# Performance work log

Hardware: AMD Instinct MI355X
Metric: run time of the kernel (lower is better)

## Reference

```python
import jax, jax.numpy as jnp
import numpy as np

BATCH, IN_F, OUT_F = 8192, 2048, 2048
LN2 = float(np.log(2.0))


def setup_inputs() -> dict:
    key = jax.random.key(0)
    kx, kw = jax.random.split(key)
    x = jax.random.normal(kx, (BATCH, IN_F), dtype=jnp.float32)
    # kaiming_uniform_(a=sqrt(5)) on (OUT_F, IN_F+1): U(-1/sqrt(fan_in), 1/sqrt(fan_in))
    bound = 1.0 / np.sqrt(IN_F + 1)
    W = jax.random.uniform(kw, (OUT_F, IN_F + 1), dtype=jnp.float32,
                           minval=-bound, maxval=bound)
    W = W.at[:, -1].set(0.0)  # bias column initialized to 0
    return {"x": x, "W": W}


def reference(x, W):
    # UniversalKANNode forward, node_type='add', use_bias=True,
    # function = lshifted_softplus: f(x, w) = w * (softplus(x) - ln2)
    # Append bias ones column: (B, IN_F+1)
    xb = jnp.concatenate([x, jnp.ones((x.shape[0], 1), dtype=x.dtype)], axis=-1)
    phi = jax.nn.softplus(xb) - jnp.asarray(LN2, dtype=x.dtype)  # (B, IN_F+1)
    # sum over input dim of W[o,i] * phi[b,i]  ==  GEMM
    return jnp.einsum("bi,oi->bo", phi, W)  # (B, OUT_F)
```

## Files before the change

kernel.cpp:

```cpp
#include <hip/hip_runtime.h>

#define M_DIM 8192
#define N_DIM 2048
#define K_DIM 2048
#define LN2F 0.69314718055994530942f
#define LOG2EF 1.44269504088896340736f
#define BIAS_PHI 0.62009741f

typedef _Float16 f16x8 __attribute__((ext_vector_type(8)));
typedef float f32x4 __attribute__((ext_vector_type(4)));

__device__ __forceinline__ float softplus_m_ln2(float v) {
    float t = v * LOG2EF;
    float e = __builtin_amdgcn_exp2f(t);
    float r = (__builtin_amdgcn_logf(1.0f + e) - 1.0f) * LN2F;
    return t < 24.0f ? r : v - LN2F;
}

__global__ __launch_bounds__(256) void prep_kernel(const float* __restrict__ x,
                                                   const float* __restrict__ W,
                                                   _Float16* __restrict__ phi,
                                                   _Float16* __restrict__ Wh,
                                                   float* __restrict__ bias) {
    if (blockIdx.x < 8192) {
        size_t i = ((size_t)blockIdx.x * blockDim.x + threadIdx.x) * 8;
        float4 v0 = *(const float4*)(x + i);
        float4 v1 = *(const float4*)(x + i + 4);
        union { _Float16 h[8]; uint4 u; } pk;
        pk.h[0] = (_Float16)softplus_m_ln2(v0.x);
        pk.h[1] = (_Float16)softplus_m_ln2(v0.y);
        pk.h[2] = (_Float16)softplus_m_ln2(v0.z);
        pk.h[3] = (_Float16)softplus_m_ln2(v0.w);
        pk.h[4] = (_Float16)softplus_m_ln2(v1.x);
        pk.h[5] = (_Float16)softplus_m_ln2(v1.y);
        pk.h[6] = (_Float16)softplus_m_ln2(v1.z);
        pk.h[7] = (_Float16)softplus_m_ln2(v1.w);
        *(uint4*)(phi + i) = pk.u;
    } else {
        const int o = blockIdx.x - 8192;
        const float* row = W + (size_t)o * (K_DIM + 1) + threadIdx.x * 8;
        union { _Float16 h[8]; uint4 u; } pk;
#pragma unroll
        for (int j = 0; j < 8; ++j)
            pk.h[j] = (_Float16)row[j];
        *(uint4*)(Wh + (size_t)o * K_DIM + threadIdx.x * 8) = pk.u;
        if (threadIdx.x == 0)
            bias[o] = W[(size_t)o * (K_DIM + 1) + K_DIM] * BIAS_PHI;
    }
}

#define GLL(gp, lp)                                                                     \
    __builtin_amdgcn_global_load_lds((const __attribute__((address_space(1))) void*)(gp), \
                                     (__attribute__((address_space(3))) void*)(lp), 16, 0, 0)

__global__ __launch_bounds__(512, 2) void kan_gemm(const _Float16* __restrict__ A,
                                                   const _Float16* __restrict__ B,
                                                   const float* __restrict__ bias,
                                                   float* __restrict__ C) {
    __shared__ __align__(16) _Float16 sA[2][256 * 64];
    __shared__ __align__(16) _Float16 sB[2][256 * 64];

    const int tid  = threadIdx.x;
    const int lane = tid & 63;
    const int wv   = tid >> 6;
    const int wm   = wv >> 2;
    const int wn   = wv & 3;

    const size_t Arow0 = (size_t)blockIdx.x * 256;
    const size_t Bcol0 = (size_t)blockIdx.y * 256;

    const int r8 = lane >> 3;
    const int lc = (lane & 7) ^ r8;
    const _Float16* gA = A + (Arow0 + wv * 32 + r8) * (size_t)K_DIM + lc * 8;
    const _Float16* gB = B + (Bcol0 + wv * 32 + r8) * (size_t)K_DIM + lc * 8;

    const int lr   = lane & 15;
    const int kph0 = ((lane >> 4) ^ (lr & 7)) * 8;

    f32x4 acc[8][4];
#pragma unroll
    for (int i = 0; i < 8; ++i)
#pragma unroll
        for (int j = 0; j < 4; ++j)
            acc[i][j] = (f32x4){0.0f, 0.0f, 0.0f, 0.0f};

#pragma unroll
    for (int j = 0; j < 4; ++j)
        GLL(gA + (size_t)j * 8 * K_DIM, &sA[0][(wv * 32 + j * 8) * 64]);
#pragma unroll
    for (int j = 0; j < 4; ++j)
        GLL(gB + (size_t)j * 8 * K_DIM, &sB[0][(wv * 32 + j * 8) * 64]);
    asm volatile("s_waitcnt vmcnt(0)" ::: "memory");
    __builtin_amdgcn_s_barrier();

    f16x8 afr[4][2];
    f16x8 bfr[2][2];

    for (int t = 0; t < 32; ++t) {
        const int d = t & 1;
        const _Float16* sAd = sA[d];
        const _Float16* sBd = sB[d];
        _Float16* dA = sA[d ^ 1];
        _Float16* dB = sB[d ^ 1];
        const size_t kn = (size_t)(t + 1) * 64;
        const bool more = (t + 1) < 32;

#pragma unroll
        for (int mi = 0; mi < 4; ++mi)
#pragma unroll
            for (int kc = 0; kc < 2; ++kc)
                afr[mi][kc] = *(const f16x8*)&sAd[(wm * 128 + mi * 16 + lr) * 64 + (kph0 ^ (kc * 32))];
#pragma unroll
        for (int ni = 0; ni < 2; ++ni)
#pragma unroll
            for (int kc = 0; kc < 2; ++kc)
                bfr[ni][kc] = *(const f16x8*)&sBd[(wn * 64 + ni * 16 + lr) * 64 + (kph0 ^ (kc * 32))];
        if (more) {
            GLL(gA + kn + (size_t)0 * 8 * K_DIM, &dA[(wv * 32 + 0) * 64]);
            GLL(gA + kn + (size_t)1 * 8 * K_DIM, &dA[(wv * 32 + 8) * 64]);
        }
        __builtin_amdgcn_s_barrier();
        asm volatile("s_waitcnt lgkmcnt(0)" ::: "memory");
        __builtin_amdgcn_s_setprio(1);
#pragma unroll
        for (int kc = 0; kc < 2; ++kc)
#pragma unroll
            for (int mi = 0; mi < 4; ++mi)
#pragma unroll
                for (int ni = 0; ni < 2; ++ni)
                    acc[mi][ni] = __builtin_amdgcn_mfma_f32_16x16x32_f16(
                        afr[mi][kc], bfr[ni][kc], acc[mi][ni], 0, 0, 0);
        __builtin_amdgcn_s_setprio(0);
        __builtin_amdgcn_s_barrier();

#pragma unroll
        for (int ni = 0; ni < 2; ++ni)
#pragma unroll
            for (int kc = 0; kc < 2; ++kc)
                bfr[ni][kc] = *(const f16x8*)&sBd[(wn * 64 + 32 + ni * 16 + lr) * 64 + (kph0 ^ (kc * 32))];
        if (more) {
            GLL(gA + kn + (size_t)2 * 8 * K_DIM, &dA[(wv * 32 + 16) * 64]);
            GLL(gA + kn + (size_t)3 * 8 * K_DIM, &dA[(wv * 32 + 24) * 64]);
        }
        __builtin_amdgcn_s_barrier();
        asm volatile("s_waitcnt lgkmcnt(0)" ::: "memory");
        __builtin_amdgcn_s_setprio(1);
#pragma unroll
        for (int kc = 0; kc < 2; ++kc)
#pragma unroll
            for (int mi = 0; mi < 4; ++mi)
#pragma unroll
                for (int ni = 0; ni < 2; ++ni)
                    acc[mi][2 + ni] = __builtin_amdgcn_mfma_f32_16x16x32_f16(
                        afr[mi][kc], bfr[ni][kc], acc[mi][2 + ni], 0, 0, 0);
        __builtin_amdgcn_s_setprio(0);
        __builtin_amdgcn_s_barrier();

#pragma unroll
        for (int mi = 0; mi < 4; ++mi)
#pragma unroll
            for (int kc = 0; kc < 2; ++kc)
                afr[mi][kc] = *(const f16x8*)&sAd[(wm * 128 + 64 + mi * 16 + lr) * 64 + (kph0 ^ (kc * 32))];
        if (more) {
            GLL(gB + kn + (size_t)0 * 8 * K_DIM, &dB[(wv * 32 + 0) * 64]);
            GLL(gB + kn + (size_t)1 * 8 * K_DIM, &dB[(wv * 32 + 8) * 64]);
        }
        __builtin_amdgcn_s_barrier();
        asm volatile("s_waitcnt lgkmcnt(0)" ::: "memory");
        __builtin_amdgcn_s_setprio(1);
#pragma unroll
        for (int kc = 0; kc < 2; ++kc)
#pragma unroll
            for (int mi = 0; mi < 4; ++mi)
#pragma unroll
                for (int ni = 0; ni < 2; ++ni)
                    acc[4 + mi][2 + ni] = __builtin_amdgcn_mfma_f32_16x16x32_f16(
                        afr[mi][kc], bfr[ni][kc], acc[4 + mi][2 + ni], 0, 0, 0);
        __builtin_amdgcn_s_setprio(0);
        __builtin_amdgcn_s_barrier();

#pragma unroll
        for (int ni = 0; ni < 2; ++ni)
#pragma unroll
            for (int kc = 0; kc < 2; ++kc)
                bfr[ni][kc] = *(const f16x8*)&sBd[(wn * 64 + ni * 16 + lr) * 64 + (kph0 ^ (kc * 32))];
        if (more) {
            GLL(gB + kn + (size_t)2 * 8 * K_DIM, &dB[(wv * 32 + 16) * 64]);
            GLL(gB + kn + (size_t)3 * 8 * K_DIM, &dB[(wv * 32 + 24) * 64]);
        }
        __builtin_amdgcn_s_barrier();
        asm volatile("s_waitcnt lgkmcnt(0)" ::: "memory");
        __builtin_amdgcn_s_setprio(1);
#pragma unroll
        for (int kc = 0; kc < 2; ++kc)
#pragma unroll
            for (int mi = 0; mi < 4; ++mi)
#pragma unroll
                for (int ni = 0; ni < 2; ++ni)
                    acc[4 + mi][ni] = __builtin_amdgcn_mfma_f32_16x16x32_f16(
                        afr[mi][kc], bfr[ni][kc], acc[4 + mi][ni], 0, 0, 0);
        __builtin_amdgcn_s_setprio(0);

        asm volatile("s_waitcnt vmcnt(0)" ::: "memory");
        __builtin_amdgcn_s_barrier();
    }

    const int crow = (lane >> 4) * 4;
    float bsv[4];
#pragma unroll
    for (int ni = 0; ni < 4; ++ni)
        bsv[ni] = bias[Bcol0 + wn * 64 + ni * 16 + lr];

#pragma unroll
    for (int mi = 0; mi < 8; ++mi) {
#pragma unroll
        for (int r = 0; r < 4; ++r) {
            float* cp = C + (Arow0 + wm * 128 + mi * 16 + crow + r) * (size_t)N_DIM
                        + Bcol0 + wn * 64 + lr;
#pragma unroll
            for (int ni = 0; ni < 4; ++ni)
                cp[ni * 16] = acc[mi][ni][r] + bsv[ni];
        }
    }
}

extern "C" void kernel_launch(void* const* d_in, const int* in_sizes, int n_in,
                              void* d_out, int out_size, void* d_ws, size_t ws_size,
                              hipStream_t stream) {
    const float* x = (const float*)d_in[0];
    const float* W = (const float*)d_in[1];
    float* out = (float*)d_out;

    char* ws = (char*)d_ws;
    _Float16* phi = (_Float16*)ws;
    _Float16* Wh  = (_Float16*)(ws + (size_t)M_DIM * K_DIM * sizeof(_Float16));
    float* bias   = (float*)(ws + (size_t)M_DIM * K_DIM * sizeof(_Float16)
                                + (size_t)N_DIM * K_DIM * sizeof(_Float16));

    prep_kernel<<<8192 + 2048, 256, 0, stream>>>(x, W, phi, Wh, bias);
    dim3 grid(M_DIM / 256, N_DIM / 256);
    kan_gemm<<<grid, 512, 0, stream>>>(phi, Wh, bias, out);
}
```

Measured before the change: 188.1 us.

## Reorder GEMM quadrant schedule and load-row assignment for finer-grained vmcnt waits

Each wave's global-to-LDS rows are reassigned to match the consumer quadrants, and the four MFMA quadrants run in a new order (A0B0, A1B0, A1B1, A0B1). Separate register fragments are kept for both A halves and both B halves. Partial vmcnt waits then replace the single full wait at the end of each k-step, and the last phase does no LDS reads, so prefetch overlaps more with compute. The cost is more VGPRs for the duplicated fragments, which could hurt occupancy under launch bounds (512,2).

```diff
diff --git a/kernel.cpp b/kernel.cpp
--- a/kernel.cpp
+++ b/kernel.cpp
@@ -71,8 +71,23 @@
 
     const int r8 = lane >> 3;
     const int lc = (lane & 7) ^ r8;
-    const _Float16* gA = A + (Arow0 + wv * 32 + r8) * (size_t)K_DIM + lc * 8;
-    const _Float16* gB = B + (Bcol0 + wv * 32 + r8) * (size_t)K_DIM + lc * 8;
+
+    const int g0 = wv * 2, g1 = wv * 2 + 1;
+    const int rA[4] = {(g0 >> 3) * 128 + (g0 & 7) * 8,
+                       (g1 >> 3) * 128 + (g1 & 7) * 8,
+                       (g0 >> 3) * 128 + (g0 & 7) * 8 + 64,
+                       (g1 >> 3) * 128 + (g1 & 7) * 8 + 64};
+    const int rB[4] = {(g0 >> 2) * 64 + (g0 & 3) * 8,
+                       (g1 >> 2) * 64 + (g1 & 3) * 8,
+                       (g0 >> 2) * 64 + (g0 & 3) * 8 + 32,
+                       (g1 >> 2) * 64 + (g1 & 3) * 8 + 32};
+    const _Float16* gAj[4];
+    const _Float16* gBj[4];
+#pragma unroll
+    for (int j = 0; j < 4; ++j) {
+        gAj[j] = A + (Arow0 + rA[j] + r8) * (size_t)K_DIM + lc * 8;
+        gBj[j] = B + (Bcol0 + rB[j] + r8) * (size_t)K_DIM + lc * 8;
+    }
 
     const int lr   = lane & 15;
     const int kph0 = ((lane >> 4) ^ (lr & 7)) * 8;
@@ -86,15 +101,15 @@
 
 #pragma unroll
     for (int j = 0; j < 4; ++j)
-        GLL(gA + (size_t)j * 8 * K_DIM, &sA[0][(wv * 32 + j * 8) * 64]);
+        GLL(gAj[j], &sA[0][rA[j] * 64]);
 #pragma unroll
     for (int j = 0; j < 4; ++j)
-        GLL(gB + (size_t)j * 8 * K_DIM, &sB[0][(wv * 32 + j * 8) * 64]);
+        GLL(gBj[j], &sB[0][rB[j] * 64]);
     asm volatile("s_waitcnt vmcnt(0)" ::: "memory");
     __builtin_amdgcn_s_barrier();
 
-    f16x8 afr[4][2];
-    f16x8 bfr[2][2];
+    f16x8 afr0[4][2], afr1[4][2];
+    f16x8 bfr0[2][2], bfr1[2][2];
 
     for (int t = 0; t < 32; ++t) {
         const int d = t & 1;
@@ -109,15 +124,15 @@
         for (int mi = 0; mi < 4; ++mi)
 #pragma unroll
             for (int kc = 0; kc < 2; ++kc)
-                afr[mi][kc] = *(const f16x8*)&sAd[(wm * 128 + mi * 16 + lr) * 64 + (kph0 ^ (kc * 32))];
+                afr0[mi][kc] = *(const f16x8*)&sAd[(wm * 128 + mi * 16 + lr) * 64 + (kph0 ^ (kc * 32))];
 #pragma unroll
         for (int ni = 0; ni < 2; ++ni)
 #pragma unroll
             for (int kc = 0; kc < 2; ++kc)
-                bfr[ni][kc] = *(const f16x8*)&sBd[(wn * 64 + ni * 16 + lr) * 64 + (kph0 ^ (kc * 32))];
-        if (more) {
-            GLL(gA + kn + (size_t)0 * 8 * K_DIM, &dA[(wv * 32 + 0) * 64]);
-            GLL(gA + kn + (size_t)1 * 8 * K_DIM, &dA[(wv * 32 + 8) * 64]);
+                bfr0[ni][kc] = *(const f16x8*)&sBd[(wn * 64 + ni * 16 + lr) * 64 + (kph0 ^ (kc * 32))];
+        if (more) {
+            GLL(gAj[0] + kn, &dA[rA[0] * 64]);
+            GLL(gAj[1] + kn, &dA[rA[1] * 64]);
         }
         __builtin_amdgcn_s_barrier();
         asm volatile("s_waitcnt lgkmcnt(0)" ::: "memory");
@@ -129,18 +144,45 @@
 #pragma unroll
                 for (int ni = 0; ni < 2; ++ni)
                     acc[mi][ni] = __builtin_amdgcn_mfma_f32_16x16x32_f16(
-                        afr[mi][kc], bfr[ni][kc], acc[mi][ni], 0, 0, 0);
-        __builtin_amdgcn_s_setprio(0);
+                        afr0[mi][kc], bfr0[ni][kc], acc[mi][ni], 0, 0, 0);
+        __builtin_amdgcn_s_setprio(0);
+        __builtin_amdgcn_s_barrier();
+
+#pragma unroll
+        for (int mi = 0; mi < 4; ++mi)
+#pragma unroll
+            for (int kc = 0; kc < 2; ++kc)
+                afr1[mi][kc] = *(const f16x8*)&sAd[(wm * 128 + 64 + mi * 16 + lr) * 64 + (kph0 ^ (kc * 32))];
+        if (more) {
+            GLL(gAj[2] + kn, &dA[rA[2] * 64]);
+            GLL(gAj[3] + kn, &dA[rA[3] * 64]);
+        }
+        __builtin_amdgcn_s_barrier();
+        asm volatile("s_waitcnt lgkmcnt(0)" ::: "memory");
+        __builtin_amdgcn_s_setprio(1);
+#pragma unroll
+        for (int kc = 0; kc < 2; ++kc)
+#pragma unroll
+            for (int mi = 0; mi < 4; ++mi)
+#pragma unroll
+                for (int ni = 0; ni < 2; ++ni)
+                    acc[4 + mi][ni] = __builtin_amdgcn_mfma_f32_16x16x32_f16(
+                        afr1[mi][kc], bfr0[ni][kc], acc[4 + mi][ni], 0, 0, 0);
+        __builtin_amdgcn_s_setprio(0);
+        if (more)
+            asm volatile("s_waitcnt vmcnt(4)" ::: "memory");
+        else
+            asm volatile("s_waitcnt vmcnt(0)" ::: "memory");
         __builtin_amdgcn_s_barrier();
 
 #pragma unroll
         for (int ni = 0; ni < 2; ++ni)
 #pragma unroll
             for (int kc = 0; kc < 2; ++kc)
-                bfr[ni][kc] = *(const f16x8*)&sBd[(wn * 64 + 32 + ni * 16 + lr) * 64 + (kph0 ^ (kc * 32))];
-        if (more) {
-            GLL(gA + kn + (size_t)2 * 8 * K_DIM, &dA[(wv * 32 + 16) * 64]);
-            GLL(gA + kn + (size_t)3 * 8 * K_DIM, &dA[(wv * 32 + 24) * 64]);
+                bfr1[ni][kc] = *(const f16x8*)&sBd[(wn * 64 + 32 + ni * 16 + lr) * 64 + (kph0 ^ (kc * 32))];
+        if (more) {
+            GLL(gBj[0] + kn, &dB[rB[0] * 64]);
+            GLL(gBj[1] + kn, &dB[rB[1] * 64]);
         }
         __builtin_amdgcn_s_barrier();
         asm volatile("s_waitcnt lgkmcnt(0)" ::: "memory");
@@ -151,75 +193,46 @@
             for (int mi = 0; mi < 4; ++mi)
 #pragma unroll
                 for (int ni = 0; ni < 2; ++ni)
+                    acc[4 + mi][2 + ni] = __builtin_amdgcn_mfma_f32_16x16x32_f16(
+                        afr1[mi][kc], bfr1[ni][kc], acc[4 + mi][2 + ni], 0, 0, 0);
+        __builtin_amdgcn_s_setprio(0);
+        __builtin_amdgcn_s_barrier();
+
+        if (more) {
+            GLL(gBj[2] + kn, &dB[rB[2] * 64]);
+            GLL(gBj[3] + kn, &dB[rB[3] * 64]);
+        }
+        __builtin_amdgcn_s_barrier();
+        __builtin_amdgcn_s_setprio(1);
+#pragma unroll
+        for (int kc = 0; kc < 2; ++kc)
+#pragma unroll
+            for (int mi = 0; mi < 4; ++mi)
+#pragma unroll
+                for (int ni = 0; ni < 2; ++ni)
                     acc[mi][2 + ni] = __builtin_amdgcn_mfma_f32_16x16x32_f16(
-                        afr[mi][kc], bfr[ni][kc], acc[mi][2 + ni], 0, 0, 0);
-        __builtin_amdgcn_s_setprio(0);
-        __builtin_amdgcn_s_barrier();
-
-#pragma unroll
-        for (int mi = 0; mi < 4; ++mi)
-#pragma unroll
-            for (int kc = 0; kc < 2; ++kc)
-                afr[mi][kc] = *(const f16x8*)&sAd[(wm * 128 + 64 + mi * 16 + lr) * 64 + (kph0 ^ (kc * 32))];
-        if (more) {
-            GLL(gB + kn + (size_t)0 * 8 * K_DIM, &dB[(wv * 32 + 0) * 64]);
-            GLL(gB + kn + (size_t)1 * 8 * K_DIM, &dB[(wv * 32 + 8) * 64]);
-        }
-        __builtin_amdgcn_s_barrier();
-        asm volatile("s_waitcnt lgkmcnt(0)" ::: "memory");
-        __builtin_amdgcn_s_setprio(1);
-#pragma unroll
-        for (int kc = 0; kc < 2; ++kc)
-#pragma unroll
-            for (int mi = 0; mi < 4; ++mi)
-#pragma unroll
-                for (int ni = 0; ni < 2; ++ni)
-                    acc[4 + mi][2 + ni] = __builtin_amdgcn_mfma_f32_16x16x32_f16(
-                        afr[mi][kc], bfr[ni][kc], acc[4 + mi][2 + ni], 0, 0, 0);
-        __builtin_amdgcn_s_setprio(0);
-        __builtin_amdgcn_s_barrier();
-
-#pragma unroll
-        for (int ni = 0; ni < 2; ++ni)
-#pragma unroll
-            for (int kc = 0; kc < 2; ++kc)
-                bfr[ni][kc] = *(const f16x8*)&sBd[(wn * 64 + ni * 16 + lr) * 64 + (kph0 ^ (kc * 32))];
-        if (more) {
-            GLL(gB + kn + (size_t)2 * 8 * K_DIM, &dB[(wv * 32 + 16) * 64]);
-            GLL(gB + kn + (size_t)3 * 8 * K_DIM, &dB[(wv * 32 + 24) * 64]);
-        }
-        __builtin_amdgcn_s_barrier();
-        asm volatile("s_waitcnt lgkmcnt(0)" ::: "memory");
-        __builtin_amdgcn_s_setprio(1);
-#pragma unroll
-        for (int kc = 0; kc < 2; ++kc)
-#pragma unroll
-            for (int mi = 0; mi < 4; ++mi)
-#pragma unroll
-                for (int ni = 0; ni < 2; ++ni)
-                    acc[4 + mi][ni] = __builtin_amdgcn_mfma_f32_16x16x32_f16(
-                        afr[mi][kc], bfr[ni][kc], acc[4 + mi][ni], 0, 0, 0);
-        __builtin_amdgcn_s_setprio(0);
-
-        asm volatile("s_waitcnt vmcnt(0)" ::: "memory");
+                        afr0[mi][kc], bfr1[ni][kc], acc[mi][2 + ni], 0, 0, 0);
+        __builtin_amdgcn_s_setprio(0);
+        if (more)
+            asm volatile("s_waitcnt vmcnt(2)" ::: "memory");
         __builtin_amdgcn_s_barrier();
     }
 
     const int crow = (lane >> 4) * 4;
     float bsv[4];
 #pragma unroll
-    for (int ni = 0; ni < 4; ++ni)
-        bsv[ni] = bias[Bcol0 + wn * 64 + ni * 16 + lr];
-
-#pragma unroll
-    for (int mi = 0; mi < 8; ++mi) {
+    for (int bj = 0; bj < 4; ++bj)
+        bsv[bj] = bias[Bcol0 + wn * 64 + (bj >> 1) * 32 + (bj & 1) * 16 + lr];
+
+#pragma unroll
+    for (int ai = 0; ai < 8; ++ai) {
 #pragma unroll
         for (int r = 0; r < 4; ++r) {
-            float* cp = C + (Arow0 + wm * 128 + mi * 16 + crow + r) * (size_t)N_DIM
+            float* cp = C + (Arow0 + wm * 128 + (ai >> 2) * 64 + (ai & 3) * 16 + crow + r) * (size_t)N_DIM
                         + Bcol0 + wn * 64 + lr;
 #pragma unroll
-            for (int ni = 0; ni < 4; ++ni)
-                cp[ni * 16] = acc[mi][ni][r] + bsv[ni];
+            for (int bj = 0; bj < 4; ++bj)
+                cp[(bj >> 1) * 32 + (bj & 1) * 16] = acc[ai][bj][r] + bsv[bj];
         }
     }
 }
```

New measurement: 185.8 us. Within noise of the previous version (-1.2%).
